# Kernel optimization log

Measured on AMD Instinct MI355X. Metric: run time of the kernel, lower is better.

## Reference

```python
import jax, jax.numpy as jnp
import numpy as np

B, T, F, U = 256, 2048, 64, 10  # batch, timesteps, features, lstm units


def setup_inputs() -> dict:
    key = jax.random.key(0)
    k1, k2, k3, k4 = jax.random.split(key, 4)
    return {
        "x": jax.random.normal(k1, (B, T, F), dtype=jnp.float32),
        "kernel": jax.random.normal(k2, (F, 4 * U), dtype=jnp.float32) * 0.1,
        "recurrent_kernel": jax.random.normal(k3, (U, 4 * U), dtype=jnp.float32) * 0.1,
        "bias": jnp.zeros((4 * U,), dtype=jnp.float32),
        "dense_w": jax.random.normal(k4, (U, 1), dtype=jnp.float32) * 0.1,
        "dense_b": jnp.zeros((1,), dtype=jnp.float32),
    }


def reference(x, kernel, recurrent_kernel, bias, dense_w, dense_b):
    units = recurrent_kernel.shape[0]
    batch = x.shape[0]
    # Precompute input contribution for all timesteps: [B, T, 4U]
    xz = jnp.einsum('btf,fg->btg', x, kernel) + bias

    def step(carry, z_t):
        h, c = carry
        z = z_t + h @ recurrent_kernel  # [B, 4U]
        i, f, g, o = jnp.split(z, 4, axis=-1)  # Keras gate order: i, f, c, o
        i = jax.nn.sigmoid(i)
        f = jax.nn.sigmoid(f)
        g = jax.nn.soft_sign(g)       # activation='softsign'
        o = jax.nn.sigmoid(o)
        c = f * c + i * g
        h = o * jax.nn.soft_sign(c)
        return (h, c), None

    h0 = jnp.zeros((batch, units), dtype=x.dtype)
    (h, _), _ = jax.lax.scan(step, (h0, h0), jnp.swapaxes(xz, 0, 1))
    logit = h @ dense_w + dense_b  # [B, 1]
    return jax.nn.sigmoid(logit)
```

## Files before the change

kernel.cpp:

```cpp
#include <hip/hip_runtime.h>

#define B_ 256
#define T_ 2048
#define F_ 64
#define U_ 10
#define G_ 40
#define CH 32
#define CH2 (CH / 2)
#define NCH (T_ / CH)
#define NLOG2E (-1.44269504088896340736f)

__device__ __forceinline__ float rcp_f(float x) { return __builtin_amdgcn_rcpf(x); }
__device__ __forceinline__ float exp2_f(float x) { return __builtin_amdgcn_exp2f(x); }
__device__ __forceinline__ float rdlane_f(float v, int l) {
  return __int_as_float(__builtin_amdgcn_readlane(__float_as_int(v), l));
}
template <int CTRL>
__device__ __forceinline__ float qbcast(float v) {
  return __int_as_float(
      __builtin_amdgcn_update_dpp(0, __float_as_int(v), CTRL, 0xF, 0xF, true));
}
__device__ __forceinline__ void gload_lds16(const float* g, float* l) {
  __builtin_amdgcn_global_load_lds(
      (const __attribute__((address_space(1))) void*)g,
      (__attribute__((address_space(3))) void*)l, 16, 0, 0);
}

__global__ __launch_bounds__(256, 1) void lstm_fused(
    const float* __restrict__ x, const float* __restrict__ W,
    const float* __restrict__ R, const float* __restrict__ bias,
    const float* __restrict__ dw, const float* __restrict__ db,
    float* __restrict__ out) {
  __shared__ float xb[2][CH * F_];
  __shared__ float2 zb[2][CH2 * G_];
  const int b = blockIdx.x;
  const int tid = threadIdx.x;
  const int wave = tid >> 6;
  const int lane = tid & 63;
  const float* xbase = x + (size_t)b * T_ * F_;

  if (wave == 0) {
    __builtin_amdgcn_s_setprio(3);
    const int L = (lane < G_) ? lane : (G_ - 1);
    const int u = L >> 2, gate = L & 3;
    const int col = gate * U_ + u;
    const float sc = (gate == 2) ? 1.f : NLOG2E;
    float Rc[U_];
    #pragma unroll
    for (int j = 0; j < U_; ++j) Rc[j] = R[j * G_ + col] * sc;
    const float dwu = dw[u];
    const float db0 = db[0];
    float h = 0.f, c = 0.f;

    auto step = [&](float zseed) {
      float h0 = rdlane_f(h, 0),  h1 = rdlane_f(h, 4),  h2 = rdlane_f(h, 8);
      float h3 = rdlane_f(h, 12), h4 = rdlane_f(h, 16), h5 = rdlane_f(h, 20);
      float h6 = rdlane_f(h, 24), h7 = rdlane_f(h, 28);
      float h8 = rdlane_f(h, 32), h9 = rdlane_f(h, 36);
      float z0 = fmaf(h0, Rc[0], zseed);
      float z1 = h1 * Rc[1];
      z0 = fmaf(h2, Rc[2], z0);  z1 = fmaf(h3, Rc[3], z1);
      z0 = fmaf(h4, Rc[4], z0);  z1 = fmaf(h5, Rc[5], z1);
      z0 = fmaf(h6, Rc[6], z0);  z1 = fmaf(h7, Rc[7], z1);
      z0 = fmaf(h8, Rc[8], z0);  z1 = fmaf(h9, Rc[9], z1);
      float zz = z0 + z1;
      float e = exp2_f(zz);
      float t = (gate == 2) ? __builtin_fabsf(zz) : e;
      float r = rcp_f(1.f + t);
      float a = (gate == 2) ? zz * r : r;
      float ai = qbcast<0x00>(a);
      float af = qbcast<0x55>(a);
      float ag = qbcast<0xAA>(a);
      float ao = qbcast<0xFF>(a);
      c = fmaf(af, c, ai * ag);
      float oc = ao * c;
      float den = 1.f + __builtin_fabsf(c);
      h = oc * rcp_f(den);
    };

    __syncthreads();
    __syncthreads();
    for (int cc = 0; cc < NCH; ++cc) {
      const float2* zp = zb[cc & 1] + L;
      float2 sd[CH2];
      #pragma unroll
      for (int k = 0; k < CH2; ++k) sd[k] = zp[k * G_];
      #pragma unroll
      for (int k = 0; k < CH2; ++k) {
        step(sd[k].x);
        step(sd[k].y);
      }
      __syncthreads();
    }
    float p = h * dwu;
    float logit = db0;
    #pragma unroll
    for (int j = 0; j < U_; ++j) logit += rdlane_f(p, 4 * j);
    if (lane == 0) out[b] = rcp_f(1.f + __expf(-logit));
  } else {
    const int p0 = tid - 64;
    const int p = (p0 < 160) ? p0 : 159;
    const bool act = (p0 < 160);
    const int s = p % G_;
    const int tp = p / G_;
    const int u = s >> 2, gate = s & 3;
    const int col = gate * U_ + u;
    const int pw = wave - 1;
    const float scp = (gate == 2) ? 1.f : NLOG2E;
    float wc[F_];
    #pragma unroll
    for (int k = 0; k < F_; ++k) wc[k] = W[k * G_ + col];
    const float bcol = bias[col];

    auto load_x = [&](int cx) {
      const float* g = xbase + (size_t)cx * CH * F_;
      float* l = xb[cx & 1];
      for (int i = pw; i < 8; i += 3)
        gload_lds16(g + i * 256 + lane * 4, l + i * 256);
    };
    auto dot = [&](const float* xr) -> float {
      const float4* row4 = (const float4*)xr;
      float z0 = bcol, z1 = 0.f, z2 = 0.f, z3 = 0.f;
      #pragma unroll
      for (int j = 0; j < 16; j += 4) {
        float4 a0 = row4[j], a1 = row4[j + 1], a2 = row4[j + 2], a3 = row4[j + 3];
        z0 = fmaf(a0.x, wc[4*j+0], z0);  z0 = fmaf(a0.y, wc[4*j+1], z0);
        z0 = fmaf(a0.z, wc[4*j+2], z0);  z0 = fmaf(a0.w, wc[4*j+3], z0);
        z1 = fmaf(a1.x, wc[4*j+4], z1);  z1 = fmaf(a1.y, wc[4*j+5], z1);
        z1 = fmaf(a1.z, wc[4*j+6], z1);  z1 = fmaf(a1.w, wc[4*j+7], z1);
        z2 = fmaf(a2.x, wc[4*j+8], z2);  z2 = fmaf(a2.y, wc[4*j+9], z2);
        z2 = fmaf(a2.z, wc[4*j+10], z2); z2 = fmaf(a2.w, wc[4*j+11], z2);
        z3 = fmaf(a3.x, wc[4*j+12], z3); z3 = fmaf(a3.y, wc[4*j+13], z3);
        z3 = fmaf(a3.z, wc[4*j+14], z3); z3 = fmaf(a3.w, wc[4*j+15], z3);
      }
      return ((z0 + z1) + (z2 + z3)) * scp;
    };
    auto produce = [&](int tc) {
      const float* xr = xb[tc & 1];
      float2* zrow = zb[tc & 1];
      #pragma unroll
      for (int k = 0; k < 4; ++k) {
        const int t2 = tp + 4 * k;
        float zE = dot(xr + (2 * t2) * F_);
        float zO = dot(xr + (2 * t2 + 1) * F_);
        if (act) zrow[t2 * G_ + s] = make_float2(zE, zO);
      }
    };

    load_x(0);
    load_x(1);
    __syncthreads();
    produce(0);
    __syncthreads();
    for (int cc = 0; cc < NCH; ++cc) {
      if (cc + 2 < NCH) load_x(cc + 2);
      if (cc + 1 < NCH) produce(cc + 1);
      __syncthreads();
    }
  }
}

extern "C" void kernel_launch(void* const* d_in, const int* in_sizes, int n_in,
                              void* d_out, int out_size, void* d_ws, size_t ws_size,
                              hipStream_t stream) {
  const float* x    = (const float*)d_in[0];
  const float* W    = (const float*)d_in[1];
  const float* R    = (const float*)d_in[2];
  const float* bias = (const float*)d_in[3];
  const float* dw   = (const float*)d_in[4];
  const float* db   = (const float*)d_in[5];
  float* out = (float*)d_out;
  (void)d_ws; (void)ws_size; (void)in_sizes; (void)n_in; (void)out_size;
  lstm_fused<<<B_, 256, 0, stream>>>(x, W, R, bias, dw, db, out);
}
```

Measured before the change: 337.2 us.

## Double chunk size, stream z-seed LDS reads, and shorten recurrent FMA chain

Doubles the timestep chunk from 32 to 64, halving the number of block-wide barriers the serial recurrent wave must wait on. The producer waves load and compute twice as many rows per chunk. The consumer now preloads half the chunk's z seeds and refills the register buffer while stepping, which keeps register pressure bounded and overlaps LDS reads with compute. The recurrent dot product is split into four shorter partial sums to cut the dependent FMA latency per step. The trade-off is larger LDS buffers and more producer work per barrier interval, which could stall the consumer if the producers fall behind.

```diff
diff --git a/kernel.cpp b/kernel.cpp
--- a/kernel.cpp
+++ b/kernel.cpp
@@ -5,8 +5,9 @@
 #define F_ 64
 #define U_ 10
 #define G_ 40
-#define CH 32
+#define CH 64
 #define CH2 (CH / 2)
+#define HB 16
 #define NCH (T_ / CH)
 #define NLOG2E (-1.44269504088896340736f)
 
@@ -57,13 +58,17 @@
       float h3 = rdlane_f(h, 12), h4 = rdlane_f(h, 16), h5 = rdlane_f(h, 20);
       float h6 = rdlane_f(h, 24), h7 = rdlane_f(h, 28);
       float h8 = rdlane_f(h, 32), h9 = rdlane_f(h, 36);
-      float z0 = fmaf(h0, Rc[0], zseed);
-      float z1 = h1 * Rc[1];
-      z0 = fmaf(h2, Rc[2], z0);  z1 = fmaf(h3, Rc[3], z1);
-      z0 = fmaf(h4, Rc[4], z0);  z1 = fmaf(h5, Rc[5], z1);
-      z0 = fmaf(h6, Rc[6], z0);  z1 = fmaf(h7, Rc[7], z1);
-      z0 = fmaf(h8, Rc[8], z0);  z1 = fmaf(h9, Rc[9], z1);
-      float zz = z0 + z1;
+      float q0 = fmaf(h0, Rc[0], zseed);
+      q0 = fmaf(h1, Rc[1], q0);
+      q0 = fmaf(h2, Rc[2], q0);
+      float q1 = h3 * Rc[3];
+      q1 = fmaf(h4, Rc[4], q1);
+      q1 = fmaf(h5, Rc[5], q1);
+      float q2 = h6 * Rc[6];
+      q2 = fmaf(h7, Rc[7], q2);
+      float q3 = h8 * Rc[8];
+      q3 = fmaf(h9, Rc[9], q3);
+      float zz = (q0 + q1) + (q2 + q3);
       float e = exp2_f(zz);
       float t = (gate == 2) ? __builtin_fabsf(zz) : e;
       float r = rcp_f(1.f + t);
@@ -82,11 +87,18 @@
     __syncthreads();
     for (int cc = 0; cc < NCH; ++cc) {
       const float2* zp = zb[cc & 1] + L;
-      float2 sd[CH2];
+      float2 sd[HB];
       #pragma unroll
-      for (int k = 0; k < CH2; ++k) sd[k] = zp[k * G_];
+      for (int k = 0; k < HB; ++k) sd[k] = zp[k * G_];
       #pragma unroll
-      for (int k = 0; k < CH2; ++k) {
+      for (int k = 0; k < HB; ++k) {
+        float2 s2 = sd[k];
+        sd[k] = zp[(k + HB) * G_];
+        step(s2.x);
+        step(s2.y);
+      }
+      #pragma unroll
+      for (int k = 0; k < HB; ++k) {
         step(sd[k].x);
         step(sd[k].y);
       }
@@ -115,7 +127,7 @@
     auto load_x = [&](int cx) {
       const float* g = xbase + (size_t)cx * CH * F_;
       float* l = xb[cx & 1];
-      for (int i = pw; i < 8; i += 3)
+      for (int i = pw; i < 16; i += 3)
         gload_lds16(g + i * 256 + lane * 4, l + i * 256);
     };
     auto dot = [&](const float* xr) -> float {
@@ -139,7 +151,7 @@
       const float* xr = xb[tc & 1];
       float2* zrow = zb[tc & 1];
       #pragma unroll
-      for (int k = 0; k < 4; ++k) {
+      for (int k = 0; k < 8; ++k) {
         const int t2 = tp + 4 * k;
         float zE = dot(xr + (2 * t2) * F_);
         float zO = dot(xr + (2 * t2 + 1) * F_);
```

Result: faster. 329.2 us (-2.4%).
